# Kernel tuning notes

Hardware: AMD Instinct MI355X
Metric: run time of the kernel (lower is better)

## Reference

```python
import jax, jax.numpy as jnp
from jax import lax
import numpy as np


def _gaussian_blur5(x):
    # x: [B,1,H,W]; torchvision gaussian_blur(kernel_size=5) default sigma = 0.3*((5-1)*0.5-1)+0.8 = 1.1
    sigma = 1.1
    r = jnp.arange(5, dtype=x.dtype) - 2.0
    k = jnp.exp(-(r * r) / (2.0 * sigma * sigma))
    k = k / k.sum()
    dn = ('NCHW', 'OIHW', 'NCHW')
    xp = jnp.pad(x, ((0, 0), (0, 0), (2, 2), (0, 0)), mode='reflect')
    x = lax.conv_general_dilated(xp, k.reshape(1, 1, 5, 1), (1, 1), 'VALID', dimension_numbers=dn)
    xp = jnp.pad(x, ((0, 0), (0, 0), (0, 0), (2, 2)), mode='reflect')
    return lax.conv_general_dilated(xp, k.reshape(1, 1, 1, 5), (1, 1), 'VALID', dimension_numbers=dn)


def setup_inputs() -> dict:
    key = jax.random.key(0)
    k1, k2, k3 = jax.random.split(key, 3)
    T, B, D, heads = 2, 32, 768, 12
    H_t, W_t, H_s, W_s = 14, 14, 96, 96
    template_patches = jax.random.normal(k1, (T, B, H_t * W_t, D), dtype=jnp.float32)
    template_annos = jax.random.uniform(k2, (T, B, 4), dtype=jnp.float32)
    search_key = jax.random.normal(k3, (B, heads, H_s * W_s + 1, D // heads), dtype=jnp.float32)
    return {'template_patches': template_patches, 'template_annos': template_annos,
            'search_key': search_key, 'H_t': H_t, 'W_t': W_t, 'H_s': H_s, 'W_s': W_s}


def reference(template_patches, template_annos, search_key, H_t, W_t, H_s, W_s):
    T, B, Nt, D = template_patches.shape
    heads = search_key.shape[1]
    hd = D // heads
    # --- vectorized patch-mask construction from normalized [x,y,w,h] boxes ---
    x1 = jnp.floor(template_annos[..., 0] * W_t).astype(jnp.int32)  # int() trunc == floor for >=0
    y1 = jnp.floor(template_annos[..., 1] * H_t).astype(jnp.int32)
    x2 = jnp.floor((template_annos[..., 0] + template_annos[..., 2]) * W_t).astype(jnp.int32)
    y2 = jnp.floor((template_annos[..., 1] + template_annos[..., 3]) * H_t).astype(jnp.int32)
    rows = jnp.arange(H_t)[None, None, :, None]
    cols = jnp.arange(W_t)[None, None, None, :]
    mask = ((rows >= y1[..., None, None]) & (rows < y2[..., None, None]) &
            (cols >= x1[..., None, None]) & (cols < x2[..., None, None]))
    mask = mask.reshape(T, B, Nt, 1).astype(template_patches.dtype)
    # --- masked-mean prototypes, averaged over templates ---
    count = mask.sum(axis=2)                                   # [T,B,1]
    protos = (template_patches * mask).sum(axis=2) / (count + 1e-6)  # [T,B,D]
    proto = protos.mean(axis=0)                                # [B,D]
    # --- per-head cross-attention scores against search keys (CLS stripped) ---
    proto_h = proto.reshape(B, heads, hd)
    skp = search_key[:, :, 1:, :]                              # [B,heads,Ns,hd]
    attn = jnp.einsum('bhd,bhnd->bhn', proto_h, skp) * (hd ** -0.5)
    track = attn.mean(axis=1).reshape(B, 1, H_s, W_s)
    track = _gaussian_blur5(track)
    prob = jax.nn.softmax(track.reshape(B, -1), axis=-1).reshape(B, H_s, W_s)
    # --- integral-image sliding-window box scoring ---
    im = jnp.cumsum(jnp.cumsum(prob, axis=-1), axis=-2)
    p = jnp.pad(im, ((0, 0), (1, 0), (1, 0)))
    Dv = p[:, H_t:, W_t:]
    Cv = p[:, H_t:, :-W_t]
    Bv = p[:, :-H_t, W_t:]
    Av = p[:, :-H_t, :-W_t]
    sum_map = Dv - Bv - Cv + Av                                # [B, H_s-H_t+1, W_s-W_t+1]
    flat = sum_map.reshape(B, -1)
    idx = jnp.argmax(flat, axis=1)
    confidence = jnp.max(flat, axis=1)
    best_y = idx // sum_map.shape[2]
    best_x = idx % sum_map.shape[2]
    win_w = jnp.full((B,), W_t, dtype=jnp.int32)
    win_h = jnp.full((B,), H_t, dtype=jnp.int32)
    return best_x, best_y, win_w, win_h, confidence, prob
```

## Files before the change

### kernel.cpp

```cpp
#include <hip/hip_runtime.h>
#include <math.h>

#define TT 2
#define BB 32
#define DD 768
#define HEADS 12
#define HD 64
#define HT 14
#define WT 14
#define HS 96
#define WS 96
#define NS (HS*WS)
#define NSK (NS+1)
#define SMW (WS-WT+1)
#define SMH (HS-HT+1)

__global__ __launch_bounds__(256) void proto_kernel(
    const float* __restrict__ patches, const float* __restrict__ annos,
    float* __restrict__ protos) {
  const int dc = blockIdx.x, t = blockIdx.y, b = blockIdx.z;
  const int d = dc * 256 + threadIdx.x;

  const float* an = annos + (t * BB + b) * 4;
  const float ax = an[0], ay = an[1], aw = an[2], ah = an[3];
  const int x1 = (int)floorf(ax * (float)WT);
  const int y1 = (int)floorf(ay * (float)HT);
  const int x2 = (int)floorf((ax + aw) * (float)WT);
  const int y2 = (int)floorf((ay + ah) * (float)HT);
  const int cx2 = min(x2, WT), cy2 = min(y2, HT);
  const int cw = max(cx2 - x1, 0), ch = max(cy2 - y1, 0);
  const float count = (float)(cw * ch);

  float s = 0.f;
  const float* base = patches + ((size_t)(t * BB + b)) * (HT*WT) * DD + d;
  for (int r = y1; r < cy2; ++r)
    for (int c = x1; c < cx2; ++c)
      s += base[(r * WT + c) * DD];

  protos[(size_t)(t * BB + b) * DD + d] = s / (count + 1e-6f);
}

__global__ __launch_bounds__(256) void attn_kernel(
    const float* __restrict__ sk, const float* __restrict__ protos,
    float* __restrict__ track) {
  __shared__ float sp[DD];
  const int b = blockIdx.y;
  const int n = blockIdx.x * 256 + threadIdx.x;

  for (int i = threadIdx.x; i < DD; i += 256)
    sp[i] = 0.5f * (protos[(size_t)b * DD + i] +
                    protos[(size_t)(BB + b) * DD + i]);
  __syncthreads();

  float acc = 0.f;
  const float* skb = sk + (size_t)b * HEADS * NSK * HD;
  #pragma unroll
  for (int h = 0; h < HEADS; ++h) {
    const float4* v = (const float4*)(skb + ((size_t)h * NSK + (n + 1)) * HD);
    const float* p = sp + h * HD;
    #pragma unroll
    for (int q = 0; q < HD / 4; ++q) {
      float4 x = v[q];
      acc += p[4*q+0]*x.x + p[4*q+1]*x.y + p[4*q+2]*x.z + p[4*q+3]*x.w;
    }
  }
  track[(size_t)b * NS + n] = acc * 0.125f / 12.0f;
}

__device__ __forceinline__ int reflect96(int p) {
  return p < 0 ? -p : (p > 95 ? 190 - p : p);
}

__global__ __launch_bounds__(256) void post_kernel(
    const float* __restrict__ track, float* __restrict__ out) {
  __shared__ float P[97 * 97];
  __shared__ float red[256];
  __shared__ int redi[256];
  const int b = blockIdx.x, tid = threadIdx.x;

  const float e2 = expf(-4.0f / (2.0f * 1.1f * 1.1f));
  const float e1 = expf(-1.0f / (2.0f * 1.1f * 1.1f));
  const float wsum = 2.f * e2 + 2.f * e1 + 1.f;
  const float w0 = e2 / wsum, w1 = e1 / wsum, w2 = 1.f / wsum;

  const float* tr = track + (size_t)b * NS;

  for (int i = tid; i < NS; i += 256) {
    const int r = i / WS, c = i % WS;
    float acc = w2 * tr[r * WS + c];
    acc += w1 * (tr[reflect96(r - 1) * WS + c] + tr[reflect96(r + 1) * WS + c]);
    acc += w0 * (tr[reflect96(r - 2) * WS + c] + tr[reflect96(r + 2) * WS + c]);
    P[r * 97 + c] = acc;
  }
  __syncthreads();

  float vals[36];
  #pragma unroll
  for (int k = 0; k < 36; ++k) {
    const int i = tid + k * 256;
    const int r = i / WS, c = i % WS;
    float acc = w2 * P[r * 97 + c];
    acc += w1 * (P[r * 97 + reflect96(c - 1)] + P[r * 97 + reflect96(c + 1)]);
    acc += w0 * (P[r * 97 + reflect96(c - 2)] + P[r * 97 + reflect96(c + 2)]);
    vals[k] = acc;
  }
  __syncthreads();

  float lm = -1e30f;
  #pragma unroll
  for (int k = 0; k < 36; ++k) lm = fmaxf(lm, vals[k]);
  red[tid] = lm; __syncthreads();
  for (int s = 128; s > 0; s >>= 1) {
    if (tid < s) red[tid] = fmaxf(red[tid], red[tid + s]);
    __syncthreads();
  }
  const float m = red[0]; __syncthreads();

  float ls = 0.f;
  #pragma unroll
  for (int k = 0; k < 36; ++k) { vals[k] = expf(vals[k] - m); ls += vals[k]; }
  red[tid] = ls; __syncthreads();
  for (int s = 128; s > 0; s >>= 1) {
    if (tid < s) red[tid] += red[tid + s];
    __syncthreads();
  }
  const float inv = 1.0f / red[0]; __syncthreads();

  float* prob_out = out + 5 * BB + (size_t)b * NS;
  #pragma unroll
  for (int k = 0; k < 36; ++k) {
    const int i = tid + k * 256;
    const int r = i / WS, c = i % WS;
    const float p = vals[k] * inv;
    prob_out[i] = p;
    P[(r + 1) * 97 + (c + 1)] = p;
  }
  for (int i = tid; i < 97; i += 256) { P[i] = 0.f; P[i * 97] = 0.f; }
  __syncthreads();

  if (tid < 96) {
    const int c = tid + 1;
    float run = P[97 + c];
    for (int r = 2; r < 97; ++r) { run += P[r * 97 + c]; P[r * 97 + c] = run; }
  }
  __syncthreads();
  if (tid < 96) {
    const int r = tid + 1;
    float run = 0.f;
    for (int c = 1; c < 97; ++c) { run += P[r * 97 + c]; P[r * 97 + c] = run; }
  }
  __syncthreads();

  float bv = -1e30f; int bi = 0x7fffffff;
  for (int i = tid; i < SMH * SMW; i += 256) {
    const int y = i / SMW, x = i % SMW;
    const float v = P[(y + HT) * 97 + (x + WT)] - P[y * 97 + (x + WT)]
                  - P[(y + HT) * 97 + x] + P[y * 97 + x];
    if (v > bv || (v == bv && i < bi)) { bv = v; bi = i; }
  }
  red[tid] = bv; redi[tid] = bi; __syncthreads();
  for (int s = 128; s > 0; s >>= 1) {
    if (tid < s) {
      const float ov = red[tid + s]; const int oi = redi[tid + s];
      if (ov > red[tid] || (ov == red[tid] && oi < redi[tid])) {
        red[tid] = ov; redi[tid] = oi;
      }
    }
    __syncthreads();
  }

  if (tid == 0) {
    const int idx = redi[0];
    out[0 * BB + b] = (float)(idx % SMW);
    out[1 * BB + b] = (float)(idx / SMW);
    out[2 * BB + b] = (float)WT;
    out[3 * BB + b] = (float)HT;
    out[4 * BB + b] = red[0];
  }
}

extern "C" void kernel_launch(void* const* d_in, const int* in_sizes, int n_in,
                              void* d_out, int out_size, void* d_ws, size_t ws_size,
                              hipStream_t stream) {
  (void)in_sizes; (void)n_in; (void)out_size; (void)ws_size;
  const float* patches = (const float*)d_in[0];
  const float* annos   = (const float*)d_in[1];
  const float* sk      = (const float*)d_in[2];
  float* ws = (float*)d_ws;
  float* protos = ws;
  float* track  = ws + (size_t)TT * BB * DD;
  float* out = (float*)d_out;

  proto_kernel<<<dim3(DD / 256, TT, BB), 256, 0, stream>>>(patches, annos, protos);
  attn_kernel<<<dim3(NS / 256, BB), 256, 0, stream>>>(sk, protos, track);
  post_kernel<<<BB, 256, 0, stream>>>(track, out);
}
```

Measured before the change: 1.249 ms.

## Coalesce search-key reads in attn kernel with 16-lane row groups and shuffle reduce

Each search-key row is now read by a 16-lane group, one float4 per lane, instead of one thread streaming a whole 256-byte row per head. Consecutive lanes therefore touch contiguous memory. The prototype slice is held in registers instead of shared memory, and the partial dot products are combined with xor shuffles. The grid grows fourfold to cover 64 rows per block. The aim is to fix the strided, uncoalesced loads in this bandwidth-bound kernel, at the cost of extra shuffle work and more blocks.

```diff
diff --git a/kernel.cpp b/kernel.cpp
--- a/kernel.cpp
+++ b/kernel.cpp
@@ -43,28 +43,44 @@
 __global__ __launch_bounds__(256) void attn_kernel(
     const float* __restrict__ sk, const float* __restrict__ protos,
     float* __restrict__ track) {
-  __shared__ float sp[DD];
   const int b = blockIdx.y;
-  const int n = blockIdx.x * 256 + threadIdx.x;
-
-  for (int i = threadIdx.x; i < DD; i += 256)
-    sp[i] = 0.5f * (protos[(size_t)b * DD + i] +
-                    protos[(size_t)(BB + b) * DD + i]);
-  __syncthreads();
-
-  float acc = 0.f;
+  const int tid = threadIdx.x;
+  const int lane16 = tid & 15;
+  const int grp = tid >> 4;
+  const int n0 = blockIdx.x * 64;
+
+  float4 pr[HEADS];
+  const float4* p0 = (const float4*)(protos + (size_t)b * DD);
+  const float4* p1 = (const float4*)(protos + (size_t)(BB + b) * DD);
+  #pragma unroll
+  for (int h = 0; h < HEADS; ++h) {
+    float4 a = p0[h * 16 + lane16];
+    float4 c = p1[h * 16 + lane16];
+    pr[h] = make_float4(0.5f * (a.x + c.x), 0.5f * (a.y + c.y),
+                        0.5f * (a.z + c.z), 0.5f * (a.w + c.w));
+  }
+
   const float* skb = sk + (size_t)b * HEADS * NSK * HD;
-  #pragma unroll
-  for (int h = 0; h < HEADS; ++h) {
-    const float4* v = (const float4*)(skb + ((size_t)h * NSK + (n + 1)) * HD);
-    const float* p = sp + h * HD;
+  float acc[4] = {0.f, 0.f, 0.f, 0.f};
+  #pragma unroll
+  for (int j = 0; j < 4; ++j) {
+    const int row = n0 + 16 * j + grp;
+    const float4* base = (const float4*)(skb + (size_t)(row + 1) * HD) + lane16;
     #pragma unroll
-    for (int q = 0; q < HD / 4; ++q) {
-      float4 x = v[q];
-      acc += p[4*q+0]*x.x + p[4*q+1]*x.y + p[4*q+2]*x.z + p[4*q+3]*x.w;
+    for (int h = 0; h < HEADS; ++h) {
+      float4 v = base[h * (NSK * HD / 4)];
+      acc[j] += v.x * pr[h].x + v.y * pr[h].y + v.z * pr[h].z + v.w * pr[h].w;
     }
   }
-  track[(size_t)b * NS + n] = acc * 0.125f / 12.0f;
+
+  #pragma unroll
+  for (int j = 0; j < 4; ++j) {
+    #pragma unroll
+    for (int s = 1; s < 16; s <<= 1)
+      acc[j] += __shfl_xor(acc[j], s, 64);
+    if (lane16 == 0)
+      track[(size_t)b * NS + n0 + 16 * j + grp] = acc[j] * (1.0f / 96.0f);
+  }
 }
 
 __device__ __forceinline__ int reflect96(int p) {
@@ -192,6 +208,6 @@
   float* out = (float*)d_out;
 
   proto_kernel<<<dim3(DD / 256, TT, BB), 256, 0, stream>>>(patches, annos, protos);
-  attn_kernel<<<dim3(NS / 256, BB), 256, 0, stream>>>(sk, protos, track);
+  attn_kernel<<<dim3(NS / 64, BB), 256, 0, stream>>>(sk, protos, track);
   post_kernel<<<BB, 256, 0, stream>>>(track, out);
 }
```

Result: faster. 1.196 ms (-4.2%).
